# Kernel tuning notes

Measured on AMD Instinct MI355X. Metric: run time of the kernel, lower is better.

## Reference

```python
import jax, jax.numpy as jnp
import numpy as np

N_NODES = 100000
N_EDGES = 800000
N_FEAT = 128
N_HID = 128
N_LAYERS = 3
N_CLASSES = 10
N_GRAPHS = 256


def setup_inputs() -> dict:
    key = jax.random.key(0)
    ks = jax.random.split(key, 6)
    x = jax.random.normal(ks[0], (N_NODES, N_FEAT), dtype=jnp.float32)
    edge_index = jax.random.randint(ks[1], (2, N_EDGES), 0, N_NODES, dtype=jnp.int64)
    batch = jnp.sort(jax.random.randint(ks[2], (N_NODES,), 0, N_GRAPHS, dtype=jnp.int64))
    # GCNConv weights: layer 0 is [num_feature, num_hidden], rest [hid, hid];
    # num_feature == num_hidden here so we stack them as [L, H, H].
    Ws = jax.random.normal(ks[3], (N_LAYERS, N_HID, N_HID), dtype=jnp.float32) * 0.05
    bs = jnp.zeros((N_LAYERS, N_HID), dtype=jnp.float32)
    Wc = jax.random.normal(ks[4], (N_HID, N_CLASSES), dtype=jnp.float32) * 0.05
    bc = jnp.zeros((N_CLASSES,), dtype=jnp.float32)
    return {"x": x, "edge_index": edge_index, "batch": batch,
            "Ws": Ws, "bs": bs, "Wc": Wc, "bc": bc}


def reference(x, edge_index, batch, Ws, bs, Wc, bc):
    n = x.shape[0]
    # PyG GCNConv: add self-loops, symmetric normalization deg^{-1/2} A deg^{-1/2}
    loop = jnp.arange(n, dtype=edge_index.dtype)
    src = jnp.concatenate([edge_index[0], loop])  # [E+N]
    dst = jnp.concatenate([edge_index[1], loop])
    deg = jax.ops.segment_sum(jnp.ones_like(src, dtype=x.dtype), dst, num_segments=n)
    dinv = jax.lax.rsqrt(deg)  # deg >= 1 due to self-loops
    norm = dinv[src] * dinv[dst]  # [E+N]

    for l in range(N_LAYERS):
        h = x @ Ws[l]  # [N, H] dense transform
        msgs = h[src] * norm[:, None]  # gather + scale, [E+N, H]
        x = jax.ops.segment_sum(msgs, dst, num_segments=n) + bs[l]
        x = jax.nn.elu(x)
        # F.dropout(training=self.training): identity in eval mode

    g = jax.ops.segment_max(x, batch, num_segments=N_GRAPHS)  # global_max_pool [G, H]
    logits = g @ Wc + bc
    return jax.nn.softmax(logits, axis=1)
```

## Files before the change

kernel.cpp:

```cpp
#include <hip/hip_runtime.h>
#include <float.h>
#include <math.h>

#define NNODES 100000
#define NEDGES 800000
#define NF 128
#define NCLASSES 10
#define NGRAPHS 256

#define NBIN 98
#define BCHUNK 4096
#define NB2 196
#define CNTS_PAD 20480
#define SCAN_CHUNK 2048

typedef __attribute__((ext_vector_type(8))) short bf16x8;
typedef __attribute__((ext_vector_type(4))) float f32x4;

__device__ inline ushort f2bf(float f) {
    unsigned u = __float_as_uint(f);
    u = u + 0x7FFFu + ((u >> 16) & 1u);
    return (ushort)(u >> 16);
}
__device__ inline float b2f(ushort h) {
    return __uint_as_float(((unsigned)h) << 16);
}
__device__ inline unsigned fenc(float f) {
    unsigned u = __float_as_uint(f);
    return ((int)u < 0) ? ~u : (u | 0x80000000u);
}
__device__ inline float fdec(unsigned s) {
    return (s & 0x80000000u) ? __uint_as_float(s ^ 0x80000000u) : __uint_as_float(~s);
}

__global__ __launch_bounds__(256) void binct_kernel(const int* __restrict__ dst,
                                                    unsigned* __restrict__ cnts, int E) {
    __shared__ unsigned lh[NBIN];
    int tid = threadIdx.x;
    if (tid < NBIN) lh[tid] = 0;
    __syncthreads();
    int e0 = blockIdx.x * BCHUNK;
    int e1 = min(e0 + BCHUNK, E);
    for (int e = e0 + tid; e < e1; e += 256)
        atomicAdd(&lh[dst[e] >> 10], 1u);
    __syncthreads();
    if (tid < NBIN) cnts[tid * NB2 + blockIdx.x] = lh[tid];
}

__global__ __launch_bounds__(256) void scanA_kernel(const unsigned* __restrict__ cnt,
                                                    unsigned* __restrict__ bsum, int N) {
    __shared__ unsigned wsum[4];
    int tid = threadIdx.x, wid = tid >> 6, lane = tid & 63;
    int base = blockIdx.x * SCAN_CHUNK + tid * 8;
    unsigned s = 0;
    if (base < N) {
        uint4 a = *(const uint4*)(cnt + base);
        uint4 b = *(const uint4*)(cnt + base + 4);
        s = a.x + a.y + a.z + a.w + b.x + b.y + b.z + b.w;
    }
    #pragma unroll
    for (int off = 32; off >= 1; off >>= 1) s += __shfl_down(s, off, 64);
    if (lane == 0) wsum[wid] = s;
    __syncthreads();
    if (tid == 0) bsum[blockIdx.x] = wsum[0] + wsum[1] + wsum[2] + wsum[3];
}

__global__ __launch_bounds__(64) void scanB_kernel(const unsigned* __restrict__ bsum,
                                                   unsigned* __restrict__ boff, int nb) {
    int lane = threadIdx.x;
    unsigned v = (lane < nb) ? bsum[lane] : 0u;
    unsigned incl = v;
    #pragma unroll
    for (int off = 1; off < 64; off <<= 1) {
        unsigned t = __shfl_up(incl, off, 64);
        if (lane >= off) incl += t;
    }
    if (lane < nb) boff[lane] = incl - v;
}

__global__ __launch_bounds__(256) void scanC_kernel(const unsigned* __restrict__ cnt,
                                                    const unsigned* __restrict__ boff,
                                                    unsigned* __restrict__ outp, int N) {
    __shared__ unsigned wsum[4];
    int tid = threadIdx.x, wid = tid >> 6, lane = tid & 63;
    int base = blockIdx.x * SCAN_CHUNK + tid * 8;
    unsigned v[8];
    unsigned s = 0;
    bool act = base < N;
    if (act) {
        uint4 a = *(const uint4*)(cnt + base);
        uint4 b = *(const uint4*)(cnt + base + 4);
        v[0] = a.x; v[1] = a.y; v[2] = a.z; v[3] = a.w;
        v[4] = b.x; v[5] = b.y; v[6] = b.z; v[7] = b.w;
        #pragma unroll
        for (int j = 0; j < 8; ++j) s += v[j];
    }
    unsigned incl = s;
    #pragma unroll
    for (int off = 1; off < 64; off <<= 1) {
        unsigned t = __shfl_up(incl, off, 64);
        if (lane >= off) incl += t;
    }
    if (lane == 63) wsum[wid] = incl;
    __syncthreads();
    unsigned woff = 0;
    for (int w = 0; w < 4; ++w) if (w < wid) woff += wsum[w];
    if (act) {
        unsigned run = incl - s + woff + boff[blockIdx.x];
        #pragma unroll
        for (int j = 0; j < 8; ++j) {
            outp[base + j] = run;
            run += v[j];
        }
    }
}

__global__ __launch_bounds__(256) void binscatter_kernel(const int* __restrict__ src,
                                                         const int* __restrict__ dst,
                                                         const unsigned* __restrict__ offs,
                                                         unsigned* __restrict__ bedge, int E) {
    __shared__ unsigned lcur[NBIN];
    int tid = threadIdx.x;
    if (tid < NBIN) lcur[tid] = offs[tid * NB2 + blockIdx.x];
    __syncthreads();
    int e0 = blockIdx.x * BCHUNK;
    int e1 = min(e0 + BCHUNK, E);
    for (int e = e0 + tid; e < e1; e += 256) {
        int d = dst[e];
        int b = d >> 10;
        unsigned pos = atomicAdd(&lcur[b], 1u);
        bedge[pos] = ((unsigned)src[e] << 10) | (unsigned)(d & 1023);
    }
}

__global__ __launch_bounds__(256) void bucket_kernel(const unsigned* __restrict__ bedge,
                                                     const unsigned* __restrict__ offs,
                                                     float* __restrict__ dinv,
                                                     unsigned* __restrict__ rowptr,
                                                     unsigned* __restrict__ csr_src, int N) {
    __shared__ unsigned lcnt[1024];
    __shared__ unsigned lcur[1024];
    __shared__ unsigned wsum[4];
    int b = blockIdx.x;
    int tid = threadIdx.x, wid = tid >> 6, lane = tid & 63;
    unsigned ebeg = offs[b * NB2], eend = offs[(b + 1) * NB2];
    lcnt[tid] = 0; lcnt[tid + 256] = 0; lcnt[tid + 512] = 0; lcnt[tid + 768] = 0;
    __syncthreads();
    for (unsigned e = ebeg + tid; e < eend; e += 256)
        atomicAdd(&lcnt[bedge[e] & 1023], 1u);
    __syncthreads();
    unsigned c[4];
    unsigned s = 0;
    #pragma unroll
    for (int j = 0; j < 4; ++j) { c[j] = lcnt[tid * 4 + j]; s += c[j]; }
    unsigned incl = s;
    #pragma unroll
    for (int off = 1; off < 64; off <<= 1) {
        unsigned t = __shfl_up(incl, off, 64);
        if (lane >= off) incl += t;
    }
    if (lane == 63) wsum[wid] = incl;
    __syncthreads();
    unsigned woff = 0;
    for (int w = 0; w < 4; ++w) if (w < wid) woff += wsum[w];
    unsigned run = (incl - s) + woff + ebeg;
    int gbase = b * 1024 + tid * 4;
    #pragma unroll
    for (int j = 0; j < 4; ++j) {
        if (gbase + j < N) {
            rowptr[gbase + j] = run;
            dinv[gbase + j] = rsqrtf((float)c[j] + 1.0f);
        }
        lcur[tid * 4 + j] = run;
        run += c[j];
    }
    if (b == NBIN - 1 && tid == 0) rowptr[N] = eend;
    __syncthreads();
    for (unsigned e = ebeg + tid; e < eend; e += 256) {
        unsigned v = bedge[e];
        unsigned pos = atomicAdd(&lcur[v & 1023], 1u);
        csr_src[pos] = v >> 10;
    }
}

__global__ __launch_bounds__(256) void wprep_kernel(const float* __restrict__ Ws,
                                                    short* __restrict__ Wf) {
    int l = blockIdx.x;
    for (int idx = threadIdx.x; idx < 16384; idx += 256) {
        int i = idx & 7;
        int lane = (idx >> 3) & 63;
        int ns = idx >> 9;
        int s = ns & 3, nt = ns >> 2;
        int k = s * 32 + (lane >> 4) * 8 + i;
        int n = nt * 16 + (lane & 15);
        Wf[l * 16384 + idx] = (short)f2bf(Ws[l * 16384 + k * NF + n]);
    }
}

template<bool L0>
__global__ __launch_bounds__(256) void gemm_mfma_kernel(const void* __restrict__ Xin,
                                                        const short* __restrict__ Wf,
                                                        ushort* __restrict__ Hb, int M) {
    __shared__ short Wl[16384];
    int tid = threadIdx.x;
    for (int i = tid; i < 2048; i += 256)
        ((float4*)Wl)[i] = ((const float4*)Wf)[i];

    int wave = tid >> 6, lane = tid & 63;
    int r = lane & 15, kg = lane >> 4;
    int rowbase = blockIdx.x * 128 + wave * 32;

    bf16x8 afrag[2][4];
    #pragma unroll
    for (int t = 0; t < 2; ++t) {
        #pragma unroll
        for (int s = 0; s < 4; ++s) {
            int row = rowbase + t * 16 + r;
            if (row > M - 1) row = M - 1;
            if (L0) {
                const float* p = (const float*)Xin + (size_t)row * NF + s * 32 + kg * 8;
                float4 u0 = *(const float4*)p;
                float4 u1 = *(const float4*)(p + 4);
                bf16x8 a;
                a[0] = (short)f2bf(u0.x); a[1] = (short)f2bf(u0.y);
                a[2] = (short)f2bf(u0.z); a[3] = (short)f2bf(u0.w);
                a[4] = (short)f2bf(u1.x); a[5] = (short)f2bf(u1.y);
                a[6] = (short)f2bf(u1.z); a[7] = (short)f2bf(u1.w);
                afrag[t][s] = a;
            } else {
                afrag[t][s] = *(const bf16x8*)((const ushort*)Xin + (size_t)row * NF + s * 32 + kg * 8);
            }
        }
    }

    f32x4 acc[2][8];
    #pragma unroll
    for (int t = 0; t < 2; ++t)
        #pragma unroll
        for (int n = 0; n < 8; ++n)
            acc[t][n] = (f32x4){0.f, 0.f, 0.f, 0.f};

    __syncthreads();
    const bf16x8* WL = (const bf16x8*)Wl;
    #pragma unroll
    for (int s = 0; s < 4; ++s) {
        #pragma unroll
        for (int n = 0; n < 8; ++n) {
            bf16x8 bfr = WL[(n * 4 + s) * 64 + lane];
            acc[0][n] = __builtin_amdgcn_mfma_f32_16x16x32_bf16(afrag[0][s], bfr, acc[0][n], 0, 0, 0);
            acc[1][n] = __builtin_amdgcn_mfma_f32_16x16x32_bf16(afrag[1][s], bfr, acc[1][n], 0, 0, 0);
        }
    }

    int r4 = kg * 4;
    #pragma unroll
    for (int t = 0; t < 2; ++t) {
        #pragma unroll
        for (int n = 0; n < 8; ++n) {
            #pragma unroll
            for (int q = 0; q < 4; ++q) {
                int row = rowbase + t * 16 + r4 + q;
                if (row < M) Hb[(size_t)row * NF + n * 16 + r] = f2bf(acc[t][n][q]);
            }
        }
    }
}

__global__ __launch_bounds__(256) void aggregate_kernel(const ushort* __restrict__ Hb,
                                                        const float* __restrict__ dinv,
                                                        const unsigned* __restrict__ rowptr,
                                                        const unsigned* __restrict__ csr_src,
                                                        const float* __restrict__ bias,
                                                        ushort* __restrict__ Xout, int N) {
    int gid = blockIdx.x * 256 + threadIdx.x;
    int node = gid >> 5;
    int lane = gid & 31;
    if (node >= N) return;
    float di = dinv[node];
    float sl = di * di;
    float4 b = ((const float4*)bias)[lane];
    ushort4 hv = *(const ushort4*)(Hb + (size_t)node * NF + lane * 4);
    float ax = fmaf(b2f(hv.x), sl, b.x);
    float ay = fmaf(b2f(hv.y), sl, b.y);
    float az = fmaf(b2f(hv.z), sl, b.z);
    float aw = fmaf(b2f(hv.w), sl, b.w);
    unsigned e = rowptr[node], end = rowptr[node + 1];
    for (; e + 4 <= end; e += 4) {
        unsigned s0 = csr_src[e + 0], s1 = csr_src[e + 1];
        unsigned s2 = csr_src[e + 2], s3 = csr_src[e + 3];
        float n0 = dinv[s0] * di, n1 = dinv[s1] * di;
        float n2 = dinv[s2] * di, n3 = dinv[s3] * di;
        ushort4 g0 = *(const ushort4*)(Hb + (size_t)s0 * NF + lane * 4);
        ushort4 g1 = *(const ushort4*)(Hb + (size_t)s1 * NF + lane * 4);
        ushort4 g2 = *(const ushort4*)(Hb + (size_t)s2 * NF + lane * 4);
        ushort4 g3 = *(const ushort4*)(Hb + (size_t)s3 * NF + lane * 4);
        ax = fmaf(b2f(g0.x), n0, ax); ay = fmaf(b2f(g0.y), n0, ay);
        az = fmaf(b2f(g0.z), n0, az); aw = fmaf(b2f(g0.w), n0, aw);
        ax = fmaf(b2f(g1.x), n1, ax); ay = fmaf(b2f(g1.y), n1, ay);
        az = fmaf(b2f(g1.z), n1, az); aw = fmaf(b2f(g1.w), n1, aw);
        ax = fmaf(b2f(g2.x), n2, ax); ay = fmaf(b2f(g2.y), n2, ay);
        az = fmaf(b2f(g2.z), n2, az); aw = fmaf(b2f(g2.w), n2, aw);
        ax = fmaf(b2f(g3.x), n3, ax); ay = fmaf(b2f(g3.y), n3, ay);
        az = fmaf(b2f(g3.z), n3, az); aw = fmaf(b2f(g3.w), n3, aw);
    }
    for (; e < end; ++e) {
        unsigned s = csr_src[e];
        float nm = dinv[s] * di;
        ushort4 g = *(const ushort4*)(Hb + (size_t)s * NF + lane * 4);
        ax = fmaf(b2f(g.x), nm, ax); ay = fmaf(b2f(g.y), nm, ay);
        az = fmaf(b2f(g.z), nm, az); aw = fmaf(b2f(g.w), nm, aw);
    }
    ax = ax > 0.f ? ax : expm1f(ax);
    ay = ay > 0.f ? ay : expm1f(ay);
    az = az > 0.f ? az : expm1f(az);
    aw = aw > 0.f ? aw : expm1f(aw);
    ushort4 o;
    o.x = f2bf(ax); o.y = f2bf(ay); o.z = f2bf(az); o.w = f2bf(aw);
    *(ushort4*)(Xout + (size_t)node * NF + lane * 4) = o;
}

__global__ __launch_bounds__(256) void pool_kernel(const ushort* __restrict__ X,
                                                   const int* __restrict__ batch,
                                                   unsigned* __restrict__ Gx, int N) {
    __shared__ int gb[256];
    int n0 = blockIdx.x * 256;
    int tid = threadIdx.x;
    {
        int n = n0 + tid;
        gb[tid] = (n < N) ? batch[n] : -1;
    }
    __syncthreads();
    int cg = tid & 31;
    int rg = tid >> 5;
    float mx = -FLT_MAX, my = -FLT_MAX, mz = -FLT_MAX, mw = -FLT_MAX;
    int curg = -1;
    for (int i = rg; i < 256; i += 8) {
        int n = n0 + i;
        if (n >= N) break;
        int g = gb[i];
        if (g != curg) {
            if (curg >= 0) {
                unsigned* p = Gx + (size_t)curg * NF + cg * 4;
                atomicMax(p + 0, fenc(mx)); atomicMax(p + 1, fenc(my));
                atomicMax(p + 2, fenc(mz)); atomicMax(p + 3, fenc(mw));
            }
            curg = g;
            mx = my = mz = mw = -FLT_MAX;
        }
        ushort4 v = *(const ushort4*)(X + (size_t)n * NF + cg * 4);
        mx = fmaxf(mx, b2f(v.x)); my = fmaxf(my, b2f(v.y));
        mz = fmaxf(mz, b2f(v.z)); mw = fmaxf(mw, b2f(v.w));
    }
    if (curg >= 0) {
        unsigned* p = Gx + (size_t)curg * NF + cg * 4;
        atomicMax(p + 0, fenc(mx)); atomicMax(p + 1, fenc(my));
        atomicMax(p + 2, fenc(mz)); atomicMax(p + 3, fenc(mw));
    }
}

__global__ __launch_bounds__(128) void classify_kernel(const unsigned* __restrict__ Gx,
                                                       const float* __restrict__ Wc,
                                                       const float* __restrict__ bc,
                                                       float* __restrict__ out) {
    __shared__ float gr[NF];
    __shared__ float lg[NCLASSES];
    int g = blockIdx.x;
    int tid = threadIdx.x;
    gr[tid] = fdec(Gx[(size_t)g * NF + tid]);
    __syncthreads();
    if (tid < NCLASSES) {
        float s = bc[tid];
        for (int k = 0; k < NF; ++k) s = fmaf(gr[k], Wc[k * NCLASSES + tid], s);
        lg[tid] = s;
    }
    __syncthreads();
    if (tid == 0) {
        float m = lg[0];
        #pragma unroll
        for (int c = 1; c < NCLASSES; ++c) m = fmaxf(m, lg[c]);
        float e[NCLASSES];
        float sum = 0.f;
        #pragma unroll
        for (int c = 0; c < NCLASSES; ++c) { e[c] = expf(lg[c] - m); sum += e[c]; }
        #pragma unroll
        for (int c = 0; c < NCLASSES; ++c) out[g * NCLASSES + c] = e[c] / sum;
    }
}

extern "C" void kernel_launch(void* const* d_in, const int* in_sizes, int n_in,
                              void* d_out, int out_size, void* d_ws, size_t ws_size,
                              hipStream_t stream) {
    const float* x     = (const float*)d_in[0];
    const int*   ei    = (const int*)d_in[1];
    const int*   batch = (const int*)d_in[2];
    const float* Ws    = (const float*)d_in[3];
    const float* bs    = (const float*)d_in[4];
    const float* Wc    = (const float*)d_in[5];
    const float* bc    = (const float*)d_in[6];
    float* out = (float*)d_out;

    const int* src = ei;
    const int* dst = ei + NEDGES;

    char* ws = (char*)d_ws;
    size_t off = 0;
    auto alloc = [&](size_t bytes) -> void* {
        off = (off + 255) & ~(size_t)255;
        void* p = ws + off;
        off += bytes;
        return p;
    };
    ushort*   B0      = (ushort*)alloc(sizeof(ushort) * (size_t)NNODES * NF);
    ushort*   B1      = (ushort*)alloc(sizeof(ushort) * (size_t)NNODES * NF);
    ushort*   Hb      = (ushort*)alloc(sizeof(ushort) * (size_t)NNODES * NF);
    float*    dinvp   = (float*)alloc(sizeof(float) * NNODES);
    unsigned* rowptr  = (unsigned*)alloc(sizeof(unsigned) * (NNODES + 1));
    unsigned* csr_src = (unsigned*)alloc(sizeof(unsigned) * NEDGES);
    unsigned* bedge   = (unsigned*)alloc(sizeof(unsigned) * NEDGES);
    unsigned* offs    = (unsigned*)alloc(sizeof(unsigned) * (CNTS_PAD + 1));
    unsigned* bsum    = (unsigned*)alloc(sizeof(unsigned) * 16);
    unsigned* boff    = (unsigned*)alloc(sizeof(unsigned) * 16);
    short*    Wf      = (short*)alloc(sizeof(short) * 3 * 16384);
    unsigned* cnts    = (unsigned*)alloc(sizeof(unsigned) * CNTS_PAD);
    unsigned* Gx      = (unsigned*)alloc(sizeof(unsigned) * NGRAPHS * NF);
    size_t zspan = (size_t)((char*)(Gx + NGRAPHS * NF) - (char*)cnts);

    hipMemsetAsync(cnts, 0, zspan, stream);
    wprep_kernel<<<3, 256, 0, stream>>>(Ws, Wf);
    binct_kernel<<<NB2, 256, 0, stream>>>(dst, cnts, NEDGES);
    scanA_kernel<<<CNTS_PAD / SCAN_CHUNK, 256, 0, stream>>>(cnts, bsum, CNTS_PAD);
    scanB_kernel<<<1, 64, 0, stream>>>(bsum, boff, CNTS_PAD / SCAN_CHUNK);
    scanC_kernel<<<CNTS_PAD / SCAN_CHUNK, 256, 0, stream>>>(cnts, boff, offs, CNTS_PAD);
    binscatter_kernel<<<NB2, 256, 0, stream>>>(src, dst, offs, bedge, NEDGES);
    bucket_kernel<<<NBIN, 256, 0, stream>>>(bedge, offs, dinvp, rowptr, csr_src, NNODES);

    int gemm_grid = (NNODES + 127) / 128;
    int agg_grid  = (NNODES * 32) / 256;

    gemm_mfma_kernel<true><<<gemm_grid, 256, 0, stream>>>(x, Wf + 0 * 16384, Hb, NNODES);
    aggregate_kernel<<<agg_grid, 256, 0, stream>>>(Hb, dinvp, rowptr, csr_src, bs + 0 * NF, B1, NNODES);
    gemm_mfma_kernel<false><<<gemm_grid, 256, 0, stream>>>(B1, Wf + 1 * 16384, Hb, NNODES);
    aggregate_kernel<<<agg_grid, 256, 0, stream>>>(Hb, dinvp, rowptr, csr_src, bs + 1 * NF, B0, NNODES);
    gemm_mfma_kernel<false><<<gemm_grid, 256, 0, stream>>>(B0, Wf + 2 * 16384, Hb, NNODES);
    aggregate_kernel<<<agg_grid, 256, 0, stream>>>(Hb, dinvp, rowptr, csr_src, bs + 2 * NF, B1, NNODES);

    pool_kernel<<<(NNODES + 255) / 256, 256, 0, stream>>>(B1, batch, Gx, NNODES);
    classify_kernel<<<NGRAPHS, 128, 0, stream>>>(Gx, Wc, bc, out);
}
```

Measured before the change: 267.5 us.

## Precompute per-edge norms and fuse max-pooling into last aggregation

Adds a norm_kernel that stores dinv[src]*dinv[dst] per CSR edge once, so the three aggregation passes read a contiguous norm array instead of doing a random dinv gather per edge. The last aggregation layer is templated to max-pool directly into the graph buffer through block-local shared-memory atomics, which removes the pool kernel and the final bf16 activation write and read. The cost is an extra 3.2MB norm array plus one more kernel launch. The shared-memory path assumes each 8-node block spans at most four graph ids and falls back to global atomics otherwise.

```diff
diff --git a/kernel.cpp b/kernel.cpp
--- a/kernel.cpp
+++ b/kernel.cpp
@@ -181,6 +181,17 @@
         unsigned pos = atomicAdd(&lcur[v & 1023], 1u);
         csr_src[pos] = v >> 10;
     }
+}
+
+__global__ __launch_bounds__(256) void norm_kernel(const unsigned* __restrict__ csr_src,
+                                                   const unsigned* __restrict__ rowptr,
+                                                   const float* __restrict__ dinv,
+                                                   float* __restrict__ csr_norm, int N) {
+    int node = blockIdx.x * 256 + threadIdx.x;
+    if (node >= N) return;
+    float di = dinv[node];
+    unsigned e = rowptr[node], end = rowptr[node + 1];
+    for (; e < end; ++e) csr_norm[e] = dinv[csr_src[e]] * di;
 }
 
 __global__ __launch_bounds__(256) void wprep_kernel(const float* __restrict__ Ws,
@@ -266,16 +277,27 @@
     }
 }
 
+template<bool LAST>
 __global__ __launch_bounds__(256) void aggregate_kernel(const ushort* __restrict__ Hb,
                                                         const float* __restrict__ dinv,
                                                         const unsigned* __restrict__ rowptr,
                                                         const unsigned* __restrict__ csr_src,
+                                                        const float* __restrict__ csr_norm,
                                                         const float* __restrict__ bias,
-                                                        ushort* __restrict__ Xout, int N) {
-    int gid = blockIdx.x * 256 + threadIdx.x;
+                                                        const int* __restrict__ batch,
+                                                        ushort* __restrict__ Xout,
+                                                        unsigned* __restrict__ Gx, int N) {
+    __shared__ unsigned lmax[4][NF];
+    __shared__ int g0s;
+    int tid = threadIdx.x;
+    int gid = blockIdx.x * 256 + tid;
     int node = gid >> 5;
     int lane = gid & 31;
-    if (node >= N) return;
+    if (LAST) {
+        if (tid == 0) g0s = batch[blockIdx.x * 8];
+        for (int i = tid; i < 4 * NF; i += 256) ((unsigned*)lmax)[i] = 0;
+        __syncthreads();
+    }
     float di = dinv[node];
     float sl = di * di;
     float4 b = ((const float4*)bias)[lane];
@@ -288,8 +310,8 @@
     for (; e + 4 <= end; e += 4) {
         unsigned s0 = csr_src[e + 0], s1 = csr_src[e + 1];
         unsigned s2 = csr_src[e + 2], s3 = csr_src[e + 3];
-        float n0 = dinv[s0] * di, n1 = dinv[s1] * di;
-        float n2 = dinv[s2] * di, n3 = dinv[s3] * di;
+        float n0 = csr_norm[e + 0], n1 = csr_norm[e + 1];
+        float n2 = csr_norm[e + 2], n3 = csr_norm[e + 3];
         ushort4 g0 = *(const ushort4*)(Hb + (size_t)s0 * NF + lane * 4);
         ushort4 g1 = *(const ushort4*)(Hb + (size_t)s1 * NF + lane * 4);
         ushort4 g2 = *(const ushort4*)(Hb + (size_t)s2 * NF + lane * 4);
@@ -305,7 +327,7 @@
     }
     for (; e < end; ++e) {
         unsigned s = csr_src[e];
-        float nm = dinv[s] * di;
+        float nm = csr_norm[e];
         ushort4 g = *(const ushort4*)(Hb + (size_t)s * NF + lane * 4);
         ax = fmaf(b2f(g.x), nm, ax); ay = fmaf(b2f(g.y), nm, ay);
         az = fmaf(b2f(g.z), nm, az); aw = fmaf(b2f(g.w), nm, aw);
@@ -314,47 +336,30 @@
     ay = ay > 0.f ? ay : expm1f(ay);
     az = az > 0.f ? az : expm1f(az);
     aw = aw > 0.f ? aw : expm1f(aw);
-    ushort4 o;
-    o.x = f2bf(ax); o.y = f2bf(ay); o.z = f2bf(az); o.w = f2bf(aw);
-    *(ushort4*)(Xout + (size_t)node * NF + lane * 4) = o;
-}
-
-__global__ __launch_bounds__(256) void pool_kernel(const ushort* __restrict__ X,
-                                                   const int* __restrict__ batch,
-                                                   unsigned* __restrict__ Gx, int N) {
-    __shared__ int gb[256];
-    int n0 = blockIdx.x * 256;
-    int tid = threadIdx.x;
-    {
-        int n = n0 + tid;
-        gb[tid] = (n < N) ? batch[n] : -1;
-    }
-    __syncthreads();
-    int cg = tid & 31;
-    int rg = tid >> 5;
-    float mx = -FLT_MAX, my = -FLT_MAX, mz = -FLT_MAX, mw = -FLT_MAX;
-    int curg = -1;
-    for (int i = rg; i < 256; i += 8) {
-        int n = n0 + i;
-        if (n >= N) break;
-        int g = gb[i];
-        if (g != curg) {
-            if (curg >= 0) {
-                unsigned* p = Gx + (size_t)curg * NF + cg * 4;
-                atomicMax(p + 0, fenc(mx)); atomicMax(p + 1, fenc(my));
-                atomicMax(p + 2, fenc(mz)); atomicMax(p + 3, fenc(mw));
-            }
-            curg = g;
-            mx = my = mz = mw = -FLT_MAX;
-        }
-        ushort4 v = *(const ushort4*)(X + (size_t)n * NF + cg * 4);
-        mx = fmaxf(mx, b2f(v.x)); my = fmaxf(my, b2f(v.y));
-        mz = fmaxf(mz, b2f(v.z)); mw = fmaxf(mw, b2f(v.w));
-    }
-    if (curg >= 0) {
-        unsigned* p = Gx + (size_t)curg * NF + cg * 4;
-        atomicMax(p + 0, fenc(mx)); atomicMax(p + 1, fenc(my));
-        atomicMax(p + 2, fenc(mz)); atomicMax(p + 3, fenc(mw));
+    if (!LAST) {
+        ushort4 o;
+        o.x = f2bf(ax); o.y = f2bf(ay); o.z = f2bf(az); o.w = f2bf(aw);
+        *(ushort4*)(Xout + (size_t)node * NF + lane * 4) = o;
+    } else {
+        unsigned e0 = fenc(ax), e1 = fenc(ay), e2 = fenc(az), e3 = fenc(aw);
+        int g = batch[node];
+        int slot = g - g0s;
+        int f0 = lane * 4;
+        if (slot < 4) {
+            atomicMax(&lmax[slot][f0 + 0], e0);
+            atomicMax(&lmax[slot][f0 + 1], e1);
+            atomicMax(&lmax[slot][f0 + 2], e2);
+            atomicMax(&lmax[slot][f0 + 3], e3);
+        } else {
+            unsigned* p = Gx + (size_t)g * NF + f0;
+            atomicMax(p + 0, e0); atomicMax(p + 1, e1);
+            atomicMax(p + 2, e2); atomicMax(p + 3, e3);
+        }
+        __syncthreads();
+        for (int i = tid; i < 4 * NF; i += 256) {
+            unsigned v = ((unsigned*)lmax)[i];
+            if (v) atomicMax(&Gx[(size_t)(g0s + (i >> 7)) * NF + (i & (NF - 1))], v);
+        }
     }
 }
 
@@ -410,19 +415,20 @@
         off += bytes;
         return p;
     };
-    ushort*   B0      = (ushort*)alloc(sizeof(ushort) * (size_t)NNODES * NF);
-    ushort*   B1      = (ushort*)alloc(sizeof(ushort) * (size_t)NNODES * NF);
-    ushort*   Hb      = (ushort*)alloc(sizeof(ushort) * (size_t)NNODES * NF);
-    float*    dinvp   = (float*)alloc(sizeof(float) * NNODES);
-    unsigned* rowptr  = (unsigned*)alloc(sizeof(unsigned) * (NNODES + 1));
-    unsigned* csr_src = (unsigned*)alloc(sizeof(unsigned) * NEDGES);
-    unsigned* bedge   = (unsigned*)alloc(sizeof(unsigned) * NEDGES);
-    unsigned* offs    = (unsigned*)alloc(sizeof(unsigned) * (CNTS_PAD + 1));
-    unsigned* bsum    = (unsigned*)alloc(sizeof(unsigned) * 16);
-    unsigned* boff    = (unsigned*)alloc(sizeof(unsigned) * 16);
-    short*    Wf      = (short*)alloc(sizeof(short) * 3 * 16384);
-    unsigned* cnts    = (unsigned*)alloc(sizeof(unsigned) * CNTS_PAD);
-    unsigned* Gx      = (unsigned*)alloc(sizeof(unsigned) * NGRAPHS * NF);
+    ushort*   B0       = (ushort*)alloc(sizeof(ushort) * (size_t)NNODES * NF);
+    ushort*   B1       = (ushort*)alloc(sizeof(ushort) * (size_t)NNODES * NF);
+    ushort*   Hb       = (ushort*)alloc(sizeof(ushort) * (size_t)NNODES * NF);
+    float*    dinvp    = (float*)alloc(sizeof(float) * NNODES);
+    unsigned* rowptr   = (unsigned*)alloc(sizeof(unsigned) * (NNODES + 1));
+    unsigned* csr_src  = (unsigned*)alloc(sizeof(unsigned) * NEDGES);
+    float*    csr_norm = (float*)alloc(sizeof(float) * NEDGES);
+    unsigned* bedge    = (unsigned*)alloc(sizeof(unsigned) * NEDGES);
+    unsigned* offs     = (unsigned*)alloc(sizeof(unsigned) * (CNTS_PAD + 1));
+    unsigned* bsum     = (unsigned*)alloc(sizeof(unsigned) * 16);
+    unsigned* boff     = (unsigned*)alloc(sizeof(unsigned) * 16);
+    short*    Wf       = (short*)alloc(sizeof(short) * 3 * 16384);
+    unsigned* cnts     = (unsigned*)alloc(sizeof(unsigned) * CNTS_PAD);
+    unsigned* Gx       = (unsigned*)alloc(sizeof(unsigned) * NGRAPHS * NF);
     size_t zspan = (size_t)((char*)(Gx + NGRAPHS * NF) - (char*)cnts);
 
     hipMemsetAsync(cnts, 0, zspan, stream);
@@ -433,17 +439,20 @@
     scanC_kernel<<<CNTS_PAD / SCAN_CHUNK, 256, 0, stream>>>(cnts, boff, offs, CNTS_PAD);
     binscatter_kernel<<<NB2, 256, 0, stream>>>(src, dst, offs, bedge, NEDGES);
     bucket_kernel<<<NBIN, 256, 0, stream>>>(bedge, offs, dinvp, rowptr, csr_src, NNODES);
+    norm_kernel<<<(NNODES + 255) / 256, 256, 0, stream>>>(csr_src, rowptr, dinvp, csr_norm, NNODES);
 
     int gemm_grid = (NNODES + 127) / 128;
     int agg_grid  = (NNODES * 32) / 256;
 
     gemm_mfma_kernel<true><<<gemm_grid, 256, 0, stream>>>(x, Wf + 0 * 16384, Hb, NNODES);
-    aggregate_kernel<<<agg_grid, 256, 0, stream>>>(Hb, dinvp, rowptr, csr_src, bs + 0 * NF, B1, NNODES);
+    aggregate_kernel<false><<<agg_grid, 256, 0, stream>>>(Hb, dinvp, rowptr, csr_src, csr_norm,
+                                                          bs + 0 * NF, batch, B1, Gx, NNODES);
     gemm_mfma_kernel<false><<<gemm_grid, 256, 0, stream>>>(B1, Wf + 1 * 16384, Hb, NNODES);
-    aggregate_kernel<<<agg_grid, 256, 0, stream>>>(Hb, dinvp, rowptr, csr_src, bs + 1 * NF, B0, NNODES);
+    aggregate_kernel<false><<<agg_grid, 256, 0, stream>>>(Hb, dinvp, rowptr, csr_src, csr_norm,
+                                                          bs + 1 * NF, batch, B0, Gx, NNODES);
     gemm_mfma_kernel<false><<<gemm_grid, 256, 0, stream>>>(B0, Wf + 2 * 16384, Hb, NNODES);
-    aggregate_kernel<<<agg_grid, 256, 0, stream>>>(Hb, dinvp, rowptr, csr_src, bs + 2 * NF, B1, NNODES);
-
-    pool_kernel<<<(NNODES + 255) / 256, 256, 0, stream>>>(B1, batch, Gx, NNODES);
+    aggregate_kernel<true><<<agg_grid, 256, 0, stream>>>(Hb, dinvp, rowptr, csr_src, csr_norm,
+                                                         bs + 2 * NF, batch, (ushort*)nullptr, Gx, NNODES);
+
     classify_kernel<<<NGRAPHS, 128, 0, stream>>>(Gx, Wc, bc, out);
 }
```

Result: faster. 258.7 us (-3.3%).

## Fuse global max pool into last aggregation and use one wave per node

Applied to the files above, without the earlier changes.

The aggregation kernel now gives each node a full 64-lane wave, with each lane handling two features, in place of a 32-thread group handling four. The last layer's aggregation is templated to compute the per-graph max pool itself, reducing through shared-memory atomics before a global atomicMax. This removes the separate pool kernel and the write and re-read of the final node features. Narrower per-lane gathers and a block-level shared reduction with barriers are added in exchange. The local slot indexing assumes the 8 nodes of a block span at most 8 graphs starting from the first node's graph.

```diff
diff --git a/kernel.cpp b/kernel.cpp
--- a/kernel.cpp
+++ b/kernel.cpp
@@ -266,95 +266,66 @@
     }
 }
 
-__global__ __launch_bounds__(256) void aggregate_kernel(const ushort* __restrict__ Hb,
+template<bool LAST>
+__global__ __launch_bounds__(512) void aggregate_kernel(const ushort* __restrict__ Hb,
                                                         const float* __restrict__ dinv,
                                                         const unsigned* __restrict__ rowptr,
                                                         const unsigned* __restrict__ csr_src,
                                                         const float* __restrict__ bias,
-                                                        ushort* __restrict__ Xout, int N) {
-    int gid = blockIdx.x * 256 + threadIdx.x;
-    int node = gid >> 5;
-    int lane = gid & 31;
-    if (node >= N) return;
+                                                        const int* __restrict__ batch,
+                                                        ushort* __restrict__ Xout,
+                                                        unsigned* __restrict__ Gx, int N) {
+    int tid = threadIdx.x;
+    int wave = tid >> 6, lane = tid & 63;
+    int node = blockIdx.x * 8 + wave;
+    int c0 = lane * 2;
     float di = dinv[node];
     float sl = di * di;
-    float4 b = ((const float4*)bias)[lane];
-    ushort4 hv = *(const ushort4*)(Hb + (size_t)node * NF + lane * 4);
+    float2 b = ((const float2*)bias)[lane];
+    ushort2 hv = *(const ushort2*)(Hb + (size_t)node * NF + c0);
     float ax = fmaf(b2f(hv.x), sl, b.x);
     float ay = fmaf(b2f(hv.y), sl, b.y);
-    float az = fmaf(b2f(hv.z), sl, b.z);
-    float aw = fmaf(b2f(hv.w), sl, b.w);
     unsigned e = rowptr[node], end = rowptr[node + 1];
     for (; e + 4 <= end; e += 4) {
         unsigned s0 = csr_src[e + 0], s1 = csr_src[e + 1];
         unsigned s2 = csr_src[e + 2], s3 = csr_src[e + 3];
         float n0 = dinv[s0] * di, n1 = dinv[s1] * di;
         float n2 = dinv[s2] * di, n3 = dinv[s3] * di;
-        ushort4 g0 = *(const ushort4*)(Hb + (size_t)s0 * NF + lane * 4);
-        ushort4 g1 = *(const ushort4*)(Hb + (size_t)s1 * NF + lane * 4);
-        ushort4 g2 = *(const ushort4*)(Hb + (size_t)s2 * NF + lane * 4);
-        ushort4 g3 = *(const ushort4*)(Hb + (size_t)s3 * NF + lane * 4);
+        ushort2 g0 = *(const ushort2*)(Hb + (size_t)s0 * NF + c0);
+        ushort2 g1 = *(const ushort2*)(Hb + (size_t)s1 * NF + c0);
+        ushort2 g2 = *(const ushort2*)(Hb + (size_t)s2 * NF + c0);
+        ushort2 g3 = *(const ushort2*)(Hb + (size_t)s3 * NF + c0);
         ax = fmaf(b2f(g0.x), n0, ax); ay = fmaf(b2f(g0.y), n0, ay);
-        az = fmaf(b2f(g0.z), n0, az); aw = fmaf(b2f(g0.w), n0, aw);
         ax = fmaf(b2f(g1.x), n1, ax); ay = fmaf(b2f(g1.y), n1, ay);
-        az = fmaf(b2f(g1.z), n1, az); aw = fmaf(b2f(g1.w), n1, aw);
         ax = fmaf(b2f(g2.x), n2, ax); ay = fmaf(b2f(g2.y), n2, ay);
-        az = fmaf(b2f(g2.z), n2, az); aw = fmaf(b2f(g2.w), n2, aw);
         ax = fmaf(b2f(g3.x), n3, ax); ay = fmaf(b2f(g3.y), n3, ay);
-        az = fmaf(b2f(g3.z), n3, az); aw = fmaf(b2f(g3.w), n3, aw);
     }
     for (; e < end; ++e) {
         unsigned s = csr_src[e];
         float nm = dinv[s] * di;
-        ushort4 g = *(const ushort4*)(Hb + (size_t)s * NF + lane * 4);
+        ushort2 g = *(const ushort2*)(Hb + (size_t)s * NF + c0);
         ax = fmaf(b2f(g.x), nm, ax); ay = fmaf(b2f(g.y), nm, ay);
-        az = fmaf(b2f(g.z), nm, az); aw = fmaf(b2f(g.w), nm, aw);
     }
     ax = ax > 0.f ? ax : expm1f(ax);
     ay = ay > 0.f ? ay : expm1f(ay);
-    az = az > 0.f ? az : expm1f(az);
-    aw = aw > 0.f ? aw : expm1f(aw);
-    ushort4 o;
-    o.x = f2bf(ax); o.y = f2bf(ay); o.z = f2bf(az); o.w = f2bf(aw);
-    *(ushort4*)(Xout + (size_t)node * NF + lane * 4) = o;
-}
-
-__global__ __launch_bounds__(256) void pool_kernel(const ushort* __restrict__ X,
-                                                   const int* __restrict__ batch,
-                                                   unsigned* __restrict__ Gx, int N) {
-    __shared__ int gb[256];
-    int n0 = blockIdx.x * 256;
-    int tid = threadIdx.x;
-    {
-        int n = n0 + tid;
-        gb[tid] = (n < N) ? batch[n] : -1;
-    }
-    __syncthreads();
-    int cg = tid & 31;
-    int rg = tid >> 5;
-    float mx = -FLT_MAX, my = -FLT_MAX, mz = -FLT_MAX, mw = -FLT_MAX;
-    int curg = -1;
-    for (int i = rg; i < 256; i += 8) {
-        int n = n0 + i;
-        if (n >= N) break;
-        int g = gb[i];
-        if (g != curg) {
-            if (curg >= 0) {
-                unsigned* p = Gx + (size_t)curg * NF + cg * 4;
-                atomicMax(p + 0, fenc(mx)); atomicMax(p + 1, fenc(my));
-                atomicMax(p + 2, fenc(mz)); atomicMax(p + 3, fenc(mw));
-            }
-            curg = g;
-            mx = my = mz = mw = -FLT_MAX;
-        }
-        ushort4 v = *(const ushort4*)(X + (size_t)n * NF + cg * 4);
-        mx = fmaxf(mx, b2f(v.x)); my = fmaxf(my, b2f(v.y));
-        mz = fmaxf(mz, b2f(v.z)); mw = fmaxf(mw, b2f(v.w));
-    }
-    if (curg >= 0) {
-        unsigned* p = Gx + (size_t)curg * NF + cg * 4;
-        atomicMax(p + 0, fenc(mx)); atomicMax(p + 1, fenc(my));
-        atomicMax(p + 2, fenc(mz)); atomicMax(p + 3, fenc(mw));
+    if constexpr (!LAST) {
+        ushort2 o;
+        o.x = f2bf(ax); o.y = f2bf(ay);
+        *(ushort2*)(Xout + (size_t)node * NF + c0) = o;
+    } else {
+        __shared__ unsigned lmax[8][NF];
+        __shared__ int g0s;
+        for (int i = tid; i < 8 * NF; i += 512) ((unsigned*)lmax)[i] = 0;
+        if (tid == 0) g0s = batch[blockIdx.x * 8];
+        __syncthreads();
+        int slot = batch[node] - g0s;
+        atomicMax(&lmax[slot][c0 + 0], fenc(ax));
+        atomicMax(&lmax[slot][c0 + 1], fenc(ay));
+        __syncthreads();
+        for (int i = tid; i < 8 * NF; i += 512) {
+            unsigned v = ((unsigned*)lmax)[i];
+            if (v) atomicMax(&Gx[(size_t)(g0s + (i >> 7)) * NF + (i & (NF - 1))], v);
+        }
     }
 }
 
@@ -435,15 +406,17 @@
     bucket_kernel<<<NBIN, 256, 0, stream>>>(bedge, offs, dinvp, rowptr, csr_src, NNODES);
 
     int gemm_grid = (NNODES + 127) / 128;
-    int agg_grid  = (NNODES * 32) / 256;
+    int agg_grid  = NNODES / 8;
 
     gemm_mfma_kernel<true><<<gemm_grid, 256, 0, stream>>>(x, Wf + 0 * 16384, Hb, NNODES);
-    aggregate_kernel<<<agg_grid, 256, 0, stream>>>(Hb, dinvp, rowptr, csr_src, bs + 0 * NF, B1, NNODES);
+    aggregate_kernel<false><<<agg_grid, 512, 0, stream>>>(Hb, dinvp, rowptr, csr_src,
+                                                          bs + 0 * NF, batch, B1, Gx, NNODES);
     gemm_mfma_kernel<false><<<gemm_grid, 256, 0, stream>>>(B1, Wf + 1 * 16384, Hb, NNODES);
-    aggregate_kernel<<<agg_grid, 256, 0, stream>>>(Hb, dinvp, rowptr, csr_src, bs + 1 * NF, B0, NNODES);
+    aggregate_kernel<false><<<agg_grid, 512, 0, stream>>>(Hb, dinvp, rowptr, csr_src,
+                                                          bs + 1 * NF, batch, B0, Gx, NNODES);
     gemm_mfma_kernel<false><<<gemm_grid, 256, 0, stream>>>(B0, Wf + 2 * 16384, Hb, NNODES);
-    aggregate_kernel<<<agg_grid, 256, 0, stream>>>(Hb, dinvp, rowptr, csr_src, bs + 2 * NF, B1, NNODES);
-
-    pool_kernel<<<(NNODES + 255) / 256, 256, 0, stream>>>(B1, batch, Gx, NNODES);
+    aggregate_kernel<true><<<agg_grid, 512, 0, stream>>>(Hb, dinvp, rowptr, csr_src,
+                                                         bs + 2 * NF, batch, (ushort*)nullptr, Gx, NNODES);
+
     classify_kernel<<<NGRAPHS, 128, 0, stream>>>(Gx, Wc, bc, out);
 }
```

Result: slower. 292.1 us (+9.2%).
